# Kernel optimization log

Measured on AMD Instinct MI355X. Metric: run time of the kernel, lower is better.

The kernel has to match this reference:

```python
import jax, jax.numpy as jnp
import numpy as np

N = 50000      # atoms
E = 800000     # edges (flat neighbor list)
ELEM = 64      # elem_fea_len
NBR = 64       # nbr_fea_len
EPS = 1e-5


def _bn(x, gamma, beta):
    # BatchNorm1d in training mode: biased batch stats over dim 0
    mean = jnp.mean(x, axis=0)
    var = jnp.mean(jnp.square(x - mean), axis=0)
    return (x - mean) * jax.lax.rsqrt(var + EPS) * gamma + beta


def setup_inputs() -> dict:
    key = jax.random.key(0)
    ks = jax.random.split(key, 8)
    atom_in_fea = jax.random.normal(ks[0], (N, ELEM), dtype=jnp.float32)
    nbr_fea = jax.random.normal(ks[1], (E, NBR), dtype=jnp.float32)
    self_fea_idx = jnp.sort(jax.random.randint(ks[2], (E,), 0, N))
    nbr_fea_idx = jax.random.randint(ks[3], (E,), 0, N)
    d_in = 2 * ELEM + NBR
    d_out = 2 * ELEM
    W = jax.random.normal(ks[4], (d_in, d_out), dtype=jnp.float32) / np.sqrt(d_in)
    b = jax.random.normal(ks[5], (d_out,), dtype=jnp.float32) * 0.01
    bn1_gamma = jnp.ones((d_out,), jnp.float32)
    bn1_beta = jnp.zeros((d_out,), jnp.float32)
    bn2_gamma = jnp.ones((ELEM,), jnp.float32)
    bn2_beta = jnp.zeros((ELEM,), jnp.float32)
    return {
        "atom_in_fea": atom_in_fea, "nbr_fea": nbr_fea,
        "self_fea_idx": self_fea_idx, "nbr_fea_idx": nbr_fea_idx,
        "W": W, "b": b,
        "bn1_gamma": bn1_gamma, "bn1_beta": bn1_beta,
        "bn2_gamma": bn2_gamma, "bn2_beta": bn2_beta,
    }


def reference(atom_in_fea, nbr_fea, self_fea_idx, nbr_fea_idx,
              W, b, bn1_gamma, bn1_beta, bn2_gamma, bn2_beta):
    n_atoms = atom_in_fea.shape[0]
    # gather endpoint features: (E, ELEM) each
    atom_self = atom_in_fea[self_fea_idx]
    atom_nbr = atom_in_fea[nbr_fea_idx]
    total = jnp.concatenate([atom_self, atom_nbr, nbr_fea], axis=1)  # (E, 2*ELEM+NBR)
    total = total @ W + b                                            # (E, 2*ELEM)
    total = _bn(total, bn1_gamma, bn1_beta)
    filter_fea, core_fea = jnp.split(total, 2, axis=1)
    nbr_msg = jax.nn.sigmoid(filter_fea) * jax.nn.softplus(core_fea)  # (E, ELEM)
    nbr_sumed = jax.ops.segment_sum(nbr_msg, self_fea_idx, num_segments=n_atoms)
    nbr_sumed = _bn(nbr_sumed, bn2_gamma, bn2_beta)
    return jax.nn.softplus(atom_in_fea + nbr_sumed)
```

## Files before the change

kernel.cpp:

```cpp
#include <hip/hip_runtime.h>
#include <hip/hip_bf16.h>

typedef unsigned short ushort_t;
typedef __attribute__((ext_vector_type(8))) short short8;
typedef __attribute__((ext_vector_type(4))) float f32x4;

constexpr int N_ATOMS = 50000;
constexpr int N_EDGES = 800000;
constexpr int ELEM    = 64;
constexpr int D_IN    = 192;
constexpr int D_OUT   = 128;
constexpr float EPS   = 1e-5f;

constexpr int NREP   = 16;

constexpr int EDGE_TILE       = 64;
constexpr int TILES_PER_BLOCK = 5;
constexpr int GEMM_BLOCKS     = N_EDGES / (EDGE_TILE * TILES_PER_BLOCK);
static_assert(N_EDGES % (EDGE_TILE * TILES_PER_BLOCK) == 0, "even split");

constexpr size_t OFF_NS   = 0;
constexpr size_t OFF_ABF  = OFF_NS   + (size_t)N_ATOMS * ELEM * 4;
constexpr size_t OFF_WT   = OFF_ABF  + (size_t)N_ATOMS * ELEM * 2;
constexpr size_t OFF_BN1  = OFF_WT   + (size_t)D_OUT * D_IN * 2;
constexpr size_t OFF_SC1  = OFF_BN1  + NREP * 256 * 4;
constexpr size_t OFF_BN2  = OFF_SC1  + 256 * 4;
constexpr size_t OFF_SC2  = OFF_BN2  + NREP * 128 * 4;

__device__ __forceinline__ ushort_t f32_to_bf16(float f) {
    unsigned int u = __float_as_uint(f);
    u = (u + 0x7fffu + ((u >> 16) & 1u)) >> 16;
    return (ushort_t)u;
}
__device__ __forceinline__ float softplus_f(float x) {
    return fmaxf(x, 0.f) + __logf(1.f + __expf(-fabsf(x)));
}
__device__ __forceinline__ unsigned pkbits(float lo, float hi) {
    __hip_bfloat162 h = __float22bfloat162_rn(make_float2(lo, hi));
    union { __hip_bfloat162 h2; unsigned u; } cv; cv.h2 = h; return cv.u;
}
__device__ __forceinline__ short8 pack8(float4 a, float4 b) {
    union { uint4 u4; short8 s8; } cv;
    cv.u4.x = pkbits(a.x, a.y); cv.u4.y = pkbits(a.z, a.w);
    cv.u4.z = pkbits(b.x, b.y); cv.u4.w = pkbits(b.z, b.w);
    return cv.s8;
}

__global__ void prep_init_kernel(const float* __restrict__ atom, const float* __restrict__ W,
                                 ushort_t* __restrict__ abf, ushort_t* __restrict__ Wt,
                                 float* __restrict__ ns,
                                 float* __restrict__ bn1r, float* __restrict__ bn2r) {
    int i = blockIdx.x * blockDim.x + threadIdx.x;
    if (i < N_ATOMS * ELEM) { abf[i] = f32_to_bf16(atom[i]); ns[i] = 0.f; }
    if (i < D_IN * D_OUT) {
        int k = i >> 7, n = i & 127;
        Wt[n * D_IN + k] = f32_to_bf16(W[i]);
    }
    if (i < NREP * 256) bn1r[i] = 0.f;
    if (i < NREP * 128) bn2r[i] = 0.f;
}

constexpr int BS_USHORTS = 4 * 6 * 64 * 8;

struct StageRegs {
    int   rs;
    uint4 vs[2], vn[2];
    float4 fa[2], fb[2];
};

__device__ __forceinline__ void stage_load(StageRegs& R,
                                           const ushort_t* __restrict__ abf,
                                           const float* __restrict__ nbrf,
                                           const int* __restrict__ sidx,
                                           const int* __restrict__ nidx,
                                           int e0, int tid) {
    const int w = tid & 63, v = tid >> 6;
    const int el = v * 16 + (w & 15);
    const int rs = sidx[e0 + el], rn = nidx[e0 + el];
    R.rs = rs;
    #pragma unroll
    for (int hf = 0; hf < 2; ++hf) {
        int h = (w >> 4) + hf * 4;
        R.vs[hf] = *(const uint4*)(abf + (size_t)rs * 64 + h * 8);
        R.vn[hf] = *(const uint4*)(abf + (size_t)rn * 64 + h * 8);
        const float* pf = nbrf + (size_t)(e0 + el) * 64 + h * 8;
        R.fa[hf] = *(const float4*)pf;
        R.fb[hf] = *(const float4*)(pf + 4);
    }
}

__device__ __forceinline__ void stage_write(ushort_t* __restrict__ Bs,
                                            const StageRegs& R, int tid) {
    const int w = tid & 63, v = tid >> 6;
    #pragma unroll
    for (int hf = 0; hf < 2; ++hf) {
        *(uint4*)&Bs[((v * 6 + 0 + hf) * 64 + w) * 8] = R.vs[hf];
        *(uint4*)&Bs[((v * 6 + 2 + hf) * 64 + w) * 8] = R.vn[hf];
        *(short8*)&Bs[((v * 6 + 4 + hf) * 64 + w) * 8] = pack8(R.fa[hf], R.fb[hf]);
    }
}

__global__ __launch_bounds__(256) void stats_kernel(
    const ushort_t* __restrict__ abf, const float* __restrict__ nbrf,
    const int* __restrict__ sidx, const int* __restrict__ nidx,
    const ushort_t* __restrict__ Wt, float* __restrict__ bn1r)
{
    __shared__ __align__(16) ushort_t Bs[2][BS_USHORTS];
    const int tid  = threadIdx.x;
    const int wave = tid >> 6, lane = tid & 63;
    const int m16  = lane & 15, quad = lane >> 4;
    const int base = blockIdx.x * TILES_PER_BLOCK * EDGE_TILE;

    short8 wfrag[2][6];
    #pragma unroll
    for (int t = 0; t < 2; ++t) {
        const ushort_t* wp = Wt + (size_t)(t * 64 + wave * 16 + m16) * D_IN + quad * 8;
        #pragma unroll
        for (int ks = 0; ks < 6; ++ks) wfrag[t][ks] = *(const short8*)(wp + ks * 32);
    }

    float s[2][4] = {{0.f,0.f,0.f,0.f},{0.f,0.f,0.f,0.f}};
    float q[2][4] = {{0.f,0.f,0.f,0.f},{0.f,0.f,0.f,0.f}};

    StageRegs R;
    stage_load(R, abf, nbrf, sidx, nidx, base, tid);
    stage_write(Bs[0], R, tid);
    __syncthreads();

    for (int t = 0; t < TILES_PER_BLOCK; ++t) {
        const int cur = t & 1;
        if (t + 1 < TILES_PER_BLOCK)
            stage_load(R, abf, nbrf, sidx, nidx, base + (t + 1) * EDGE_TILE, tid);

        #pragma unroll
        for (int gg = 0; gg < 4; ++gg) {
            short8 bf[6];
            #pragma unroll
            for (int ks = 0; ks < 6; ++ks)
                bf[ks] = *(const short8*)&Bs[cur][((gg * 6 + ks) * 64 + lane) * 8];

            f32x4 acc0 = {0.f,0.f,0.f,0.f}, acc1 = {0.f,0.f,0.f,0.f};
            #pragma unroll
            for (int ks = 0; ks < 6; ++ks) {
                acc0 = __builtin_amdgcn_mfma_f32_16x16x32_bf16(wfrag[0][ks], bf[ks], acc0, 0, 0, 0);
                acc1 = __builtin_amdgcn_mfma_f32_16x16x32_bf16(wfrag[1][ks], bf[ks], acc1, 0, 0, 0);
            }
            #pragma unroll
            for (int r = 0; r < 4; ++r) {
                float v0 = acc0[r], v1 = acc1[r];
                s[0][r] += v0; q[0][r] += v0 * v0;
                s[1][r] += v1; q[1][r] += v1 * v1;
            }
        }

        if (t + 1 < TILES_PER_BLOCK) stage_write(Bs[cur ^ 1], R, tid);
        __syncthreads();
    }

    float* rep = bn1r + (size_t)(blockIdx.x & (NREP - 1)) * 256;
    #pragma unroll
    for (int t = 0; t < 2; ++t)
        #pragma unroll
        for (int r = 0; r < 4; ++r) {
            float sv = s[t][r], qv = q[t][r];
            #pragma unroll
            for (int d = 1; d < 16; d <<= 1) {
                sv += __shfl_xor(sv, d);
                qv += __shfl_xor(qv, d);
            }
            if (m16 == 0) {
                int c = t * 64 + wave * 16 + quad * 4 + r;
                atomicAdd(&rep[c], sv);
                atomicAdd(&rep[128 + c], qv);
            }
        }
}

__global__ void bn1_finalize(const float* __restrict__ bn1r,
                             const float* __restrict__ g1, const float* __restrict__ b1,
                             float* __restrict__ sc) {
    int c = threadIdx.x;
    float s = 0.f, q = 0.f;
    #pragma unroll
    for (int r = 0; r < NREP; ++r) { s += bn1r[r * 256 + c]; q += bn1r[r * 256 + 128 + c]; }
    float mean = s * (1.f / N_EDGES);
    float var  = q * (1.f / N_EDGES) - mean * mean;
    float scale = g1[c] * rsqrtf(var + EPS);
    sc[c] = scale;
    sc[128 + c] = b1[c] - mean * scale;
}

__global__ __launch_bounds__(256) void msg_kernel(
    const ushort_t* __restrict__ abf, const float* __restrict__ nbrf,
    const int* __restrict__ sidx, const int* __restrict__ nidx,
    const ushort_t* __restrict__ Wt, const float* __restrict__ sc,
    float* __restrict__ ns)
{
    __shared__ __align__(16) ushort_t Bs[2][BS_USHORTS];
    __shared__ int ss[2][EDGE_TILE];
    const int tid  = threadIdx.x;
    const int wave = tid >> 6, lane = tid & 63;
    const int m16  = lane & 15, quad = lane >> 4;
    const int base = blockIdx.x * TILES_PER_BLOCK * EDGE_TILE;

    short8 wfrag[2][6];
    #pragma unroll
    for (int t = 0; t < 2; ++t) {
        const ushort_t* wp = Wt + (size_t)(t * 64 + wave * 16 + m16) * D_IN + quad * 8;
        #pragma unroll
        for (int ks = 0; ks < 6; ++ks) wfrag[t][ks] = *(const short8*)(wp + ks * 32);
    }

    float scf[4], shf[4], scc[4], shc[4];
    #pragma unroll
    for (int r = 0; r < 4; ++r) {
        int cf = wave * 16 + quad * 4 + r;
        scf[r] = sc[cf];       shf[r] = sc[128 + cf];
        scc[r] = sc[64 + cf];  shc[r] = sc[192 + cf];
    }

    StageRegs R;
    stage_load(R, abf, nbrf, sidx, nidx, base, tid);
    stage_write(Bs[0], R, tid);
    if (quad == 0) ss[0][wave * 16 + m16] = R.rs;
    __syncthreads();

    for (int t = 0; t < TILES_PER_BLOCK; ++t) {
        const int cur = t & 1;
        if (t + 1 < TILES_PER_BLOCK)
            stage_load(R, abf, nbrf, sidx, nidx, base + (t + 1) * EDGE_TILE, tid);

        #pragma unroll
        for (int gg = 0; gg < 4; ++gg) {
            short8 bf[6];
            #pragma unroll
            for (int ks = 0; ks < 6; ++ks)
                bf[ks] = *(const short8*)&Bs[cur][((gg * 6 + ks) * 64 + lane) * 8];

            f32x4 acc0 = {0.f,0.f,0.f,0.f}, acc1 = {0.f,0.f,0.f,0.f};
            #pragma unroll
            for (int ks = 0; ks < 6; ++ks) {
                acc0 = __builtin_amdgcn_mfma_f32_16x16x32_bf16(wfrag[0][ks], bf[ks], acc0, 0, 0, 0);
                acc1 = __builtin_amdgcn_mfma_f32_16x16x32_bf16(wfrag[1][ks], bf[ks], acc1, 0, 0, 0);
            }

            float m[4];
            #pragma unroll
            for (int r = 0; r < 4; ++r) {
                float yf = fmaf(acc0[r], scf[r], shf[r]);
                float yc = fmaf(acc1[r], scc[r], shc[r]);
                m[r] = softplus_f(yc) / (1.f + __expf(-yf));
            }

            int a = ss[cur][gg * 16 + m16];
            #pragma unroll
            for (int d = 1; d < 16; d <<= 1) {
                int   au = __shfl_up(a,    d, 16);
                float u0 = __shfl_up(m[0], d, 16);
                float u1 = __shfl_up(m[1], d, 16);
                float u2 = __shfl_up(m[2], d, 16);
                float u3 = __shfl_up(m[3], d, 16);
                if (m16 >= d && au == a) { m[0] += u0; m[1] += u1; m[2] += u2; m[3] += u3; }
            }
            int an = __shfl_down(a, 1, 16);
            if (m16 == 15 || an != a) {
                float* p = ns + (size_t)a * 64 + wave * 16 + quad * 4;
                atomicAdd(p + 0, m[0]); atomicAdd(p + 1, m[1]);
                atomicAdd(p + 2, m[2]); atomicAdd(p + 3, m[3]);
            }
        }

        if (t + 1 < TILES_PER_BLOCK) {
            stage_write(Bs[cur ^ 1], R, tid);
            if (quad == 0) ss[cur ^ 1][wave * 16 + m16] = R.rs;
        }
        __syncthreads();
    }
}

__global__ __launch_bounds__(256) void bn2_stats_kernel(
    const float* __restrict__ ns, float* __restrict__ bn2r)
{
    int c = threadIdx.x & 63;
    float s = 0.f, q = 0.f;
    for (int a = blockIdx.x * 4 + (threadIdx.x >> 6); a < N_ATOMS; a += 4096) {
        float v = ns[a * ELEM + c];
        s += v; q += v * v;
    }
    float* rep = bn2r + (size_t)(blockIdx.x & (NREP - 1)) * 128;
    atomicAdd(&rep[c], s);
    atomicAdd(&rep[64 + c], q);
}

__global__ void bn2_finalize(const float* __restrict__ bn2r,
                             const float* __restrict__ g2, const float* __restrict__ b2,
                             float* __restrict__ sc2) {
    int c = threadIdx.x;
    float s = 0.f, q = 0.f;
    #pragma unroll
    for (int r = 0; r < NREP; ++r) { s += bn2r[r * 128 + c]; q += bn2r[r * 128 + 64 + c]; }
    float mean = s * (1.f / N_ATOMS);
    float var  = q * (1.f / N_ATOMS) - mean * mean;
    float scale = g2[c] * rsqrtf(var + EPS);
    sc2[c] = scale;
    sc2[64 + c] = b2[c] - mean * scale;
}

__global__ void final_kernel(const float* __restrict__ atom, const float* __restrict__ ns,
                             const float* __restrict__ sc2, float* __restrict__ out)
{
    int i = blockIdx.x * blockDim.x + threadIdx.x;
    if (i < N_ATOMS * ELEM) {
        int c = i & 63;
        float x = atom[i] + fmaf(ns[i], sc2[c], sc2[64 + c]);
        out[i] = softplus_f(x);
    }
}

extern "C" void kernel_launch(void* const* d_in, const int* in_sizes, int n_in,
                              void* d_out, int out_size, void* d_ws, size_t ws_size,
                              hipStream_t stream) {
    const float* atom = (const float*)d_in[0];
    const float* nbrf = (const float*)d_in[1];
    const int*   sidx = (const int*)d_in[2];
    const int*   nidx = (const int*)d_in[3];
    const float* W    = (const float*)d_in[4];
    const float* g1   = (const float*)d_in[6];
    const float* b1   = (const float*)d_in[7];
    const float* g2   = (const float*)d_in[8];
    const float* b2   = (const float*)d_in[9];
    float* out = (float*)d_out;
    char*  ws  = (char*)d_ws;

    float*    ns   = (float*)(ws + OFF_NS);
    ushort_t* abf  = (ushort_t*)(ws + OFF_ABF);
    ushort_t* Wt   = (ushort_t*)(ws + OFF_WT);
    float*    bn1r = (float*)(ws + OFF_BN1);
    float*    sc1  = (float*)(ws + OFF_SC1);
    float*    bn2r = (float*)(ws + OFF_BN2);
    float*    sc2  = (float*)(ws + OFF_SC2);

    hipLaunchKernelGGL(prep_init_kernel, dim3((N_ATOMS * ELEM + 255) / 256), dim3(256), 0, stream,
                       atom, W, abf, Wt, ns, bn1r, bn2r);
    hipLaunchKernelGGL(stats_kernel, dim3(GEMM_BLOCKS), dim3(256), 0, stream,
                       abf, nbrf, sidx, nidx, Wt, bn1r);
    hipLaunchKernelGGL(bn1_finalize, dim3(1), dim3(128), 0, stream, bn1r, g1, b1, sc1);
    hipLaunchKernelGGL(msg_kernel, dim3(GEMM_BLOCKS), dim3(256), 0, stream,
                       abf, nbrf, sidx, nidx, Wt, sc1, ns);
    hipLaunchKernelGGL(bn2_stats_kernel, dim3(1024), dim3(256), 0, stream, ns, bn2r);
    hipLaunchKernelGGL(bn2_finalize, dim3(1), dim3(64), 0, stream, bn2r, g2, b2, sc2);
    hipLaunchKernelGGL(final_kernel, dim3((N_ATOMS * ELEM + 255) / 256), dim3(256), 0, stream,
                       atom, ns, sc2, out);
}
```

Measured before the change: 508.7 us.

## Cache GEMM output in bf16 from stats pass instead of recomputing in message pass

The stats kernel now writes the pre-BatchNorm GEMM result, packed as bf16 filter/core pairs, to a workspace buffer. A new lightweight message kernel reads that buffer with coalesced loads, applies the BN1 affine, the gate and the segmented reduction, and no longer re-gathers atom features, rereads edge features or reruns MFMA. This trades a second random-gather plus GEMM pass for a large streaming write and read of the intermediate. It also quantizes the pre-BN values to bf16.

New measurement: 539.4 us. 1.06x slower.

```diff
diff --git a/kernel.cpp b/kernel.cpp
--- a/kernel.cpp
+++ b/kernel.cpp
@@ -18,6 +18,11 @@
 constexpr int TILES_PER_BLOCK = 5;
 constexpr int GEMM_BLOCKS     = N_EDGES / (EDGE_TILE * TILES_PER_BLOCK);
 static_assert(N_EDGES % (EDGE_TILE * TILES_PER_BLOCK) == 0, "even split");
+
+constexpr int NGROUPS        = N_EDGES / 16;
+constexpr int MSG_BLOCKS     = 2500;
+constexpr int GROUPS_PER_MSG = NGROUPS / MSG_BLOCKS;
+static_assert(NGROUPS % MSG_BLOCKS == 0, "even split");
 
 constexpr size_t OFF_NS   = 0;
 constexpr size_t OFF_ABF  = OFF_NS   + (size_t)N_ATOMS * ELEM * 4;
@@ -26,6 +31,7 @@
 constexpr size_t OFF_SC1  = OFF_BN1  + NREP * 256 * 4;
 constexpr size_t OFF_BN2  = OFF_SC1  + 256 * 4;
 constexpr size_t OFF_SC2  = OFF_BN2  + NREP * 128 * 4;
+constexpr size_t OFF_U    = (OFF_SC2 + 128 * 4 + 255) & ~(size_t)255;
 
 __device__ __forceinline__ ushort_t f32_to_bf16(float f) {
     unsigned int u = __float_as_uint(f);
@@ -63,7 +69,6 @@
 constexpr int BS_USHORTS = 4 * 6 * 64 * 8;
 
 struct StageRegs {
-    int   rs;
     uint4 vs[2], vn[2];
     float4 fa[2], fb[2];
 };
@@ -77,7 +82,6 @@
     const int w = tid & 63, v = tid >> 6;
     const int el = v * 16 + (w & 15);
     const int rs = sidx[e0 + el], rn = nidx[e0 + el];
-    R.rs = rs;
     #pragma unroll
     for (int hf = 0; hf < 2; ++hf) {
         int h = (w >> 4) + hf * 4;
@@ -103,13 +107,15 @@
 __global__ __launch_bounds__(256) void stats_kernel(
     const ushort_t* __restrict__ abf, const float* __restrict__ nbrf,
     const int* __restrict__ sidx, const int* __restrict__ nidx,
-    const ushort_t* __restrict__ Wt, float* __restrict__ bn1r)
+    const ushort_t* __restrict__ Wt, float* __restrict__ bn1r,
+    unsigned* __restrict__ U)
 {
     __shared__ __align__(16) ushort_t Bs[2][BS_USHORTS];
     const int tid  = threadIdx.x;
     const int wave = tid >> 6, lane = tid & 63;
     const int m16  = lane & 15, quad = lane >> 4;
     const int base = blockIdx.x * TILES_PER_BLOCK * EDGE_TILE;
+    const int gbase = blockIdx.x * TILES_PER_BLOCK * 4;
 
     short8 wfrag[2][6];
     #pragma unroll
@@ -151,6 +157,11 @@
                 s[0][r] += v0; q[0][r] += v0 * v0;
                 s[1][r] += v1; q[1][r] += v1 * v1;
             }
+            uint4 pk;
+            pk.x = pkbits(acc0[0], acc1[0]); pk.y = pkbits(acc0[1], acc1[1]);
+            pk.z = pkbits(acc0[2], acc1[2]); pk.w = pkbits(acc0[3], acc1[3]);
+            const int g = gbase + t * 4 + gg;
+            *(uint4*)(U + (((size_t)g * 4 + wave) * 64 + lane) * 4) = pk;
         }
 
         if (t + 1 < TILES_PER_BLOCK) stage_write(Bs[cur ^ 1], R, tid);
@@ -190,26 +201,13 @@
     sc[128 + c] = b1[c] - mean * scale;
 }
 
-__global__ __launch_bounds__(256) void msg_kernel(
-    const ushort_t* __restrict__ abf, const float* __restrict__ nbrf,
-    const int* __restrict__ sidx, const int* __restrict__ nidx,
-    const ushort_t* __restrict__ Wt, const float* __restrict__ sc,
-    float* __restrict__ ns)
+__global__ __launch_bounds__(256) void msg_lite_kernel(
+    const unsigned* __restrict__ U, const int* __restrict__ sidx,
+    const float* __restrict__ sc, float* __restrict__ ns)
 {
-    __shared__ __align__(16) ushort_t Bs[2][BS_USHORTS];
-    __shared__ int ss[2][EDGE_TILE];
     const int tid  = threadIdx.x;
     const int wave = tid >> 6, lane = tid & 63;
     const int m16  = lane & 15, quad = lane >> 4;
-    const int base = blockIdx.x * TILES_PER_BLOCK * EDGE_TILE;
-
-    short8 wfrag[2][6];
-    #pragma unroll
-    for (int t = 0; t < 2; ++t) {
-        const ushort_t* wp = Wt + (size_t)(t * 64 + wave * 16 + m16) * D_IN + quad * 8;
-        #pragma unroll
-        for (int ks = 0; ks < 6; ++ks) wfrag[t][ks] = *(const short8*)(wp + ks * 32);
-    }
 
     float scf[4], shf[4], scc[4], shc[4];
     #pragma unroll
@@ -219,62 +217,43 @@
         scc[r] = sc[64 + cf];  shc[r] = sc[192 + cf];
     }
 
-    StageRegs R;
-    stage_load(R, abf, nbrf, sidx, nidx, base, tid);
-    stage_write(Bs[0], R, tid);
-    if (quad == 0) ss[0][wave * 16 + m16] = R.rs;
-    __syncthreads();
-
-    for (int t = 0; t < TILES_PER_BLOCK; ++t) {
-        const int cur = t & 1;
-        if (t + 1 < TILES_PER_BLOCK)
-            stage_load(R, abf, nbrf, sidx, nidx, base + (t + 1) * EDGE_TILE, tid);
-
-        #pragma unroll
-        for (int gg = 0; gg < 4; ++gg) {
-            short8 bf[6];
-            #pragma unroll
-            for (int ks = 0; ks < 6; ++ks)
-                bf[ks] = *(const short8*)&Bs[cur][((gg * 6 + ks) * 64 + lane) * 8];
-
-            f32x4 acc0 = {0.f,0.f,0.f,0.f}, acc1 = {0.f,0.f,0.f,0.f};
-            #pragma unroll
-            for (int ks = 0; ks < 6; ++ks) {
-                acc0 = __builtin_amdgcn_mfma_f32_16x16x32_bf16(wfrag[0][ks], bf[ks], acc0, 0, 0, 0);
-                acc1 = __builtin_amdgcn_mfma_f32_16x16x32_bf16(wfrag[1][ks], bf[ks], acc1, 0, 0, 0);
-            }
-
-            float m[4];
-            #pragma unroll
-            for (int r = 0; r < 4; ++r) {
-                float yf = fmaf(acc0[r], scf[r], shf[r]);
-                float yc = fmaf(acc1[r], scc[r], shc[r]);
-                m[r] = softplus_f(yc) / (1.f + __expf(-yf));
-            }
-
-            int a = ss[cur][gg * 16 + m16];
-            #pragma unroll
-            for (int d = 1; d < 16; d <<= 1) {
-                int   au = __shfl_up(a,    d, 16);
-                float u0 = __shfl_up(m[0], d, 16);
-                float u1 = __shfl_up(m[1], d, 16);
-                float u2 = __shfl_up(m[2], d, 16);
-                float u3 = __shfl_up(m[3], d, 16);
-                if (m16 >= d && au == a) { m[0] += u0; m[1] += u1; m[2] += u2; m[3] += u3; }
-            }
-            int an = __shfl_down(a, 1, 16);
-            if (m16 == 15 || an != a) {
-                float* p = ns + (size_t)a * 64 + wave * 16 + quad * 4;
-                atomicAdd(p + 0, m[0]); atomicAdd(p + 1, m[1]);
-                atomicAdd(p + 2, m[2]); atomicAdd(p + 3, m[3]);
-            }
-        }
-
-        if (t + 1 < TILES_PER_BLOCK) {
-            stage_write(Bs[cur ^ 1], R, tid);
-            if (quad == 0) ss[cur ^ 1][wave * 16 + m16] = R.rs;
-        }
-        __syncthreads();
+    const int g0 = blockIdx.x * GROUPS_PER_MSG;
+    const uint4* up = (const uint4*)U + ((size_t)g0 * 4 + wave) * 64 + lane;
+    const int*   sp = sidx + g0 * 16 + m16;
+
+    for (int gi = 0; gi < GROUPS_PER_MSG; ++gi) {
+        int a = *sp;
+        uint4 pk = *up;
+
+        float m[4];
+        #pragma unroll
+        for (int r = 0; r < 4; ++r) {
+            unsigned u = (&pk.x)[r];
+            float f = __uint_as_float(u << 16);
+            float c = __uint_as_float(u & 0xffff0000u);
+            float yf = fmaf(f, scf[r], shf[r]);
+            float yc = fmaf(c, scc[r], shc[r]);
+            m[r] = softplus_f(yc) * __builtin_amdgcn_rcpf(1.f + __expf(-yf));
+        }
+
+        #pragma unroll
+        for (int d = 1; d < 16; d <<= 1) {
+            int   au = __shfl_up(a,    d, 16);
+            float u0 = __shfl_up(m[0], d, 16);
+            float u1 = __shfl_up(m[1], d, 16);
+            float u2 = __shfl_up(m[2], d, 16);
+            float u3 = __shfl_up(m[3], d, 16);
+            if (m16 >= d && au == a) { m[0] += u0; m[1] += u1; m[2] += u2; m[3] += u3; }
+        }
+        int an = __shfl_down(a, 1, 16);
+        if (m16 == 15 || an != a) {
+            float* p = ns + (size_t)a * 64 + wave * 16 + quad * 4;
+            atomicAdd(p + 0, m[0]); atomicAdd(p + 1, m[1]);
+            atomicAdd(p + 2, m[2]); atomicAdd(p + 3, m[3]);
+        }
+
+        up += 4 * 64;
+        sp += 16;
     }
 }
 
@@ -339,14 +318,15 @@
     float*    sc1  = (float*)(ws + OFF_SC1);
     float*    bn2r = (float*)(ws + OFF_BN2);
     float*    sc2  = (float*)(ws + OFF_SC2);
+    unsigned* U    = (unsigned*)(ws + OFF_U);
 
     hipLaunchKernelGGL(prep_init_kernel, dim3((N_ATOMS * ELEM + 255) / 256), dim3(256), 0, stream,
                        atom, W, abf, Wt, ns, bn1r, bn2r);
     hipLaunchKernelGGL(stats_kernel, dim3(GEMM_BLOCKS), dim3(256), 0, stream,
-                       abf, nbrf, sidx, nidx, Wt, bn1r);
+                       abf, nbrf, sidx, nidx, Wt, bn1r, U);
     hipLaunchKernelGGL(bn1_finalize, dim3(1), dim3(128), 0, stream, bn1r, g1, b1, sc1);
-    hipLaunchKernelGGL(msg_kernel, dim3(GEMM_BLOCKS), dim3(256), 0, stream,
-                       abf, nbrf, sidx, nidx, Wt, sc1, ns);
+    hipLaunchKernelGGL(msg_lite_kernel, dim3(MSG_BLOCKS), dim3(256), 0, stream,
+                       U, sidx, sc1, ns);
     hipLaunchKernelGGL(bn2_stats_kernel, dim3(1024), dim3(256), 0, stream, ns, bn2r);
     hipLaunchKernelGGL(bn2_finalize, dim3(1), dim3(64), 0, stream, bn2r, g2, b2, sc2);
     hipLaunchKernelGGL(final_kernel, dim3((N_ATOMS * ELEM + 255) / 256), dim3(256), 0, stream,
```

## Pre-convert edge features to bf16 and feed MFMA directly from global memory

Applied to the files above, without the earlier changes.

Adds a pass in the prep kernel that converts nbr_fea to a bf16 workspace copy. The stats and message kernels then load edge-feature fragments straight from global memory into MFMA operands instead of staging them through LDS. The change also reads self indices directly instead of from shared memory, adds an occupancy hint to launch bounds, and replaces a divide with a fast reciprocal. Total memory traffic may rise, because the fp32 tensor is still read once and a bf16 copy is written and then read twice.

After: 654.4 us. 1.29x slower.

```diff
diff --git a/kernel.cpp b/kernel.cpp
--- a/kernel.cpp
+++ b/kernel.cpp
@@ -26,6 +26,7 @@
 constexpr size_t OFF_SC1  = OFF_BN1  + NREP * 256 * 4;
 constexpr size_t OFF_BN2  = OFF_SC1  + 256 * 4;
 constexpr size_t OFF_SC2  = OFF_BN2  + NREP * 128 * 4;
+constexpr size_t OFF_NBF  = (OFF_SC2 + 128 * 4 + 255) & ~(size_t)255;
 
 __device__ __forceinline__ ushort_t f32_to_bf16(float f) {
     unsigned int u = __float_as_uint(f);
@@ -46,9 +47,10 @@
     return cv.s8;
 }
 
-__global__ void prep_init_kernel(const float* __restrict__ atom, const float* __restrict__ W,
-                                 ushort_t* __restrict__ abf, ushort_t* __restrict__ Wt,
-                                 float* __restrict__ ns,
+__global__ void prep_init_kernel(const float* __restrict__ atom, const float* __restrict__ nbrf,
+                                 const float* __restrict__ W,
+                                 ushort_t* __restrict__ abf, ushort_t* __restrict__ nbf,
+                                 ushort_t* __restrict__ Wt, float* __restrict__ ns,
                                  float* __restrict__ bn1r, float* __restrict__ bn2r) {
     int i = blockIdx.x * blockDim.x + threadIdx.x;
     if (i < N_ATOMS * ELEM) { abf[i] = f32_to_bf16(atom[i]); ns[i] = 0.f; }
@@ -58,19 +60,24 @@
     }
     if (i < NREP * 256) bn1r[i] = 0.f;
     if (i < NREP * 128) bn2r[i] = 0.f;
-}
-
-constexpr int BS_USHORTS = 4 * 6 * 64 * 8;
+    const int stride = gridDim.x * blockDim.x;
+    for (int j = i; j < N_EDGES * 8; j += stride) {
+        const float* p = nbrf + (size_t)j * 8;
+        float4 a = *(const float4*)p;
+        float4 b = *(const float4*)(p + 4);
+        *(short8*)(nbf + (size_t)j * 8) = pack8(a, b);
+    }
+}
+
+constexpr int BS_USHORTS = 4 * 4 * 64 * 8;
 
 struct StageRegs {
     int   rs;
     uint4 vs[2], vn[2];
-    float4 fa[2], fb[2];
 };
 
 __device__ __forceinline__ void stage_load(StageRegs& R,
                                            const ushort_t* __restrict__ abf,
-                                           const float* __restrict__ nbrf,
                                            const int* __restrict__ sidx,
                                            const int* __restrict__ nidx,
                                            int e0, int tid) {
@@ -83,9 +90,6 @@
         int h = (w >> 4) + hf * 4;
         R.vs[hf] = *(const uint4*)(abf + (size_t)rs * 64 + h * 8);
         R.vn[hf] = *(const uint4*)(abf + (size_t)rn * 64 + h * 8);
-        const float* pf = nbrf + (size_t)(e0 + el) * 64 + h * 8;
-        R.fa[hf] = *(const float4*)pf;
-        R.fb[hf] = *(const float4*)(pf + 4);
     }
 }
 
@@ -94,14 +98,13 @@
     const int w = tid & 63, v = tid >> 6;
     #pragma unroll
     for (int hf = 0; hf < 2; ++hf) {
-        *(uint4*)&Bs[((v * 6 + 0 + hf) * 64 + w) * 8] = R.vs[hf];
-        *(uint4*)&Bs[((v * 6 + 2 + hf) * 64 + w) * 8] = R.vn[hf];
-        *(short8*)&Bs[((v * 6 + 4 + hf) * 64 + w) * 8] = pack8(R.fa[hf], R.fb[hf]);
-    }
-}
-
-__global__ __launch_bounds__(256) void stats_kernel(
-    const ushort_t* __restrict__ abf, const float* __restrict__ nbrf,
+        *(uint4*)&Bs[((v * 4 + 0 + hf) * 64 + w) * 8] = R.vs[hf];
+        *(uint4*)&Bs[((v * 4 + 2 + hf) * 64 + w) * 8] = R.vn[hf];
+    }
+}
+
+__global__ __launch_bounds__(256, 4) void stats_kernel(
+    const ushort_t* __restrict__ abf, const ushort_t* __restrict__ nbf,
     const int* __restrict__ sidx, const int* __restrict__ nidx,
     const ushort_t* __restrict__ Wt, float* __restrict__ bn1r)
 {
@@ -123,28 +126,44 @@
     float q[2][4] = {{0.f,0.f,0.f,0.f},{0.f,0.f,0.f,0.f}};
 
     StageRegs R;
-    stage_load(R, abf, nbrf, sidx, nidx, base, tid);
+    stage_load(R, abf, sidx, nidx, base, tid);
     stage_write(Bs[0], R, tid);
     __syncthreads();
 
     for (int t = 0; t < TILES_PER_BLOCK; ++t) {
         const int cur = t & 1;
+        const int e0 = base + t * EDGE_TILE;
         if (t + 1 < TILES_PER_BLOCK)
-            stage_load(R, abf, nbrf, sidx, nidx, base + (t + 1) * EDGE_TILE, tid);
+            stage_load(R, abf, sidx, nidx, e0 + EDGE_TILE, tid);
+
+        const ushort_t* nb = nbf + (size_t)(e0 + m16) * 64 + quad * 8;
+        short8 nA = *(const short8*)nb;
+        short8 nB = *(const short8*)(nb + 32);
 
         #pragma unroll
         for (int gg = 0; gg < 4; ++gg) {
-            short8 bf[6];
-            #pragma unroll
-            for (int ks = 0; ks < 6; ++ks)
-                bf[ks] = *(const short8*)&Bs[cur][((gg * 6 + ks) * 64 + lane) * 8];
+            short8 cA = nA, cB = nB;
+            if (gg < 3) {
+                const ushort_t* nb2 = nbf + (size_t)(e0 + (gg + 1) * 16 + m16) * 64 + quad * 8;
+                nA = *(const short8*)nb2;
+                nB = *(const short8*)(nb2 + 32);
+            }
+            short8 bf[4];
+            #pragma unroll
+            for (int ks = 0; ks < 4; ++ks)
+                bf[ks] = *(const short8*)&Bs[cur][((gg * 4 + ks) * 64 + lane) * 8];
 
             f32x4 acc0 = {0.f,0.f,0.f,0.f}, acc1 = {0.f,0.f,0.f,0.f};
             #pragma unroll
-            for (int ks = 0; ks < 6; ++ks) {
+            for (int ks = 0; ks < 4; ++ks) {
                 acc0 = __builtin_amdgcn_mfma_f32_16x16x32_bf16(wfrag[0][ks], bf[ks], acc0, 0, 0, 0);
                 acc1 = __builtin_amdgcn_mfma_f32_16x16x32_bf16(wfrag[1][ks], bf[ks], acc1, 0, 0, 0);
             }
+            acc0 = __builtin_amdgcn_mfma_f32_16x16x32_bf16(wfrag[0][4], cA, acc0, 0, 0, 0);
+            acc1 = __builtin_amdgcn_mfma_f32_16x16x32_bf16(wfrag[1][4], cA, acc1, 0, 0, 0);
+            acc0 = __builtin_amdgcn_mfma_f32_16x16x32_bf16(wfrag[0][5], cB, acc0, 0, 0, 0);
+            acc1 = __builtin_amdgcn_mfma_f32_16x16x32_bf16(wfrag[1][5], cB, acc1, 0, 0, 0);
+
             #pragma unroll
             for (int r = 0; r < 4; ++r) {
                 float v0 = acc0[r], v1 = acc1[r];
@@ -190,14 +209,13 @@
     sc[128 + c] = b1[c] - mean * scale;
 }
 
-__global__ __launch_bounds__(256) void msg_kernel(
-    const ushort_t* __restrict__ abf, const float* __restrict__ nbrf,
+__global__ __launch_bounds__(256, 4) void msg_kernel(
+    const ushort_t* __restrict__ abf, const ushort_t* __restrict__ nbf,
     const int* __restrict__ sidx, const int* __restrict__ nidx,
     const ushort_t* __restrict__ Wt, const float* __restrict__ sc,
     float* __restrict__ ns)
 {
     __shared__ __align__(16) ushort_t Bs[2][BS_USHORTS];
-    __shared__ int ss[2][EDGE_TILE];
     const int tid  = threadIdx.x;
     const int wave = tid >> 6, lane = tid & 63;
     const int m16  = lane & 15, quad = lane >> 4;
@@ -220,39 +238,55 @@
     }
 
     StageRegs R;
-    stage_load(R, abf, nbrf, sidx, nidx, base, tid);
+    stage_load(R, abf, sidx, nidx, base, tid);
     stage_write(Bs[0], R, tid);
-    if (quad == 0) ss[0][wave * 16 + m16] = R.rs;
     __syncthreads();
 
     for (int t = 0; t < TILES_PER_BLOCK; ++t) {
         const int cur = t & 1;
+        const int e0 = base + t * EDGE_TILE;
         if (t + 1 < TILES_PER_BLOCK)
-            stage_load(R, abf, nbrf, sidx, nidx, base + (t + 1) * EDGE_TILE, tid);
+            stage_load(R, abf, sidx, nidx, e0 + EDGE_TILE, tid);
+
+        const ushort_t* nb = nbf + (size_t)(e0 + m16) * 64 + quad * 8;
+        short8 nA = *(const short8*)nb;
+        short8 nB = *(const short8*)(nb + 32);
+        int    aN = sidx[e0 + m16];
 
         #pragma unroll
         for (int gg = 0; gg < 4; ++gg) {
-            short8 bf[6];
-            #pragma unroll
-            for (int ks = 0; ks < 6; ++ks)
-                bf[ks] = *(const short8*)&Bs[cur][((gg * 6 + ks) * 64 + lane) * 8];
+            short8 cA = nA, cB = nB;
+            int a = aN;
+            if (gg < 3) {
+                const ushort_t* nb2 = nbf + (size_t)(e0 + (gg + 1) * 16 + m16) * 64 + quad * 8;
+                nA = *(const short8*)nb2;
+                nB = *(const short8*)(nb2 + 32);
+                aN = sidx[e0 + (gg + 1) * 16 + m16];
+            }
+            short8 bf[4];
+            #pragma unroll
+            for (int ks = 0; ks < 4; ++ks)
+                bf[ks] = *(const short8*)&Bs[cur][((gg * 4 + ks) * 64 + lane) * 8];
 
             f32x4 acc0 = {0.f,0.f,0.f,0.f}, acc1 = {0.f,0.f,0.f,0.f};
             #pragma unroll
-            for (int ks = 0; ks < 6; ++ks) {
+            for (int ks = 0; ks < 4; ++ks) {
                 acc0 = __builtin_amdgcn_mfma_f32_16x16x32_bf16(wfrag[0][ks], bf[ks], acc0, 0, 0, 0);
                 acc1 = __builtin_amdgcn_mfma_f32_16x16x32_bf16(wfrag[1][ks], bf[ks], acc1, 0, 0, 0);
             }
+            acc0 = __builtin_amdgcn_mfma_f32_16x16x32_bf16(wfrag[0][4], cA, acc0, 0, 0, 0);
+            acc1 = __builtin_amdgcn_mfma_f32_16x16x32_bf16(wfrag[1][4], cA, acc1, 0, 0, 0);
+            acc0 = __builtin_amdgcn_mfma_f32_16x16x32_bf16(wfrag[0][5], cB, acc0, 0, 0, 0);
+            acc1 = __builtin_amdgcn_mfma_f32_16x16x32_bf16(wfrag[1][5], cB, acc1, 0, 0, 0);
 
             float m[4];
             #pragma unroll
             for (int r = 0; r < 4; ++r) {
                 float yf = fmaf(acc0[r], scf[r], shf[r]);
                 float yc = fmaf(acc1[r], scc[r], shc[r]);
-                m[r] = softplus_f(yc) / (1.f + __expf(-yf));
-            }
-
-            int a = ss[cur][gg * 16 + m16];
+                m[r] = softplus_f(yc) * __builtin_amdgcn_rcpf(1.f + __expf(-yf));
+            }
+
             #pragma unroll
             for (int d = 1; d < 16; d <<= 1) {
                 int   au = __shfl_up(a,    d, 16);
@@ -270,10 +304,7 @@
             }
         }
 
-        if (t + 1 < TILES_PER_BLOCK) {
-            stage_write(Bs[cur ^ 1], R, tid);
-            if (quad == 0) ss[cur ^ 1][wave * 16 + m16] = R.rs;
-        }
+        if (t + 1 < TILES_PER_BLOCK) stage_write(Bs[cur ^ 1], R, tid);
         __syncthreads();
     }
 }
@@ -339,14 +370,15 @@
     float*    sc1  = (float*)(ws + OFF_SC1);
     float*    bn2r = (float*)(ws + OFF_BN2);
     float*    sc2  = (float*)(ws + OFF_SC2);
+    ushort_t* nbf  = (ushort_t*)(ws + OFF_NBF);
 
     hipLaunchKernelGGL(prep_init_kernel, dim3((N_ATOMS * ELEM + 255) / 256), dim3(256), 0, stream,
-                       atom, W, abf, Wt, ns, bn1r, bn2r);
+                       atom, nbrf, W, abf, nbf, Wt, ns, bn1r, bn2r);
     hipLaunchKernelGGL(stats_kernel, dim3(GEMM_BLOCKS), dim3(256), 0, stream,
-                       abf, nbrf, sidx, nidx, Wt, bn1r);
+                       abf, nbf, sidx, nidx, Wt, bn1r);
     hipLaunchKernelGGL(bn1_finalize, dim3(1), dim3(128), 0, stream, bn1r, g1, b1, sc1);
     hipLaunchKernelGGL(msg_kernel, dim3(GEMM_BLOCKS), dim3(256), 0, stream,
-                       abf, nbrf, sidx, nidx, Wt, sc1, ns);
+                       abf, nbf, sidx, nidx, Wt, sc1, ns);
     hipLaunchKernelGGL(bn2_stats_kernel, dim3(1024), dim3(256), 0, stream, ns, bn2r);
     hipLaunchKernelGGL(bn2_finalize, dim3(1), dim3(64), 0, stream, bn2r, g2, b2, sc2);
     hipLaunchKernelGGL(final_kernel, dim3((N_ATOMS * ELEM + 255) / 256), dim3(256), 0, stream,
```
